# Performance work log

Measured on AMD Instinct MI355X. Metric: run time of the kernel, lower is better.

## Reference

```python
import jax, jax.numpy as jnp
import numpy as np

D_MODEL = 256
NUM_HEADS = 8
NUM_KV_HEADS = 4
HEAD_DIM = D_MODEL // NUM_HEADS
EPS = 1e-5


def layer_norm(x, g, b):
    mu = jnp.mean(x, axis=-1, keepdims=True)
    var = jnp.var(x, axis=-1, keepdims=True)
    return (x - mu) * jax.lax.rsqrt(var + EPS) * g + b


def gqa(x_q, x_kv, Wq, bq, Wk, bk, Wv, bv, Wo, bo):
    # x_q, x_kv: [BC, S, D]
    BC, S, D = x_q.shape
    G = NUM_HEADS // NUM_KV_HEADS
    q = (x_q @ Wq + bq).reshape(BC, S, NUM_HEADS, HEAD_DIM)
    k = (x_kv @ Wk + bk).reshape(BC, S, NUM_KV_HEADS, HEAD_DIM)
    v = (x_kv @ Wv + bv).reshape(BC, S, NUM_KV_HEADS, HEAD_DIM)
    # repeat_interleave over head dim to expand KV heads to query heads
    k = jnp.repeat(k, G, axis=2)
    v = jnp.repeat(v, G, axis=2)
    scale = 1.0 / np.sqrt(HEAD_DIM).astype(np.float32)
    scores = jnp.einsum('bqhd,bkhd->bhqk', q, k) * scale  # [BC,H,S,S]
    attn = jax.nn.softmax(scores, axis=-1)
    out = jnp.einsum('bhqk,bkhd->bqhd', attn, v).reshape(BC, S, D)
    return out @ Wo + bo


def _make_params(key):
    ks = jax.random.split(key, 20)
    D, Dkv = D_MODEL, NUM_KV_HEADS * HEAD_DIM
    s = 1.0 / np.sqrt(D).astype(np.float32)
    p = {}
    # 4 LayerNorms
    for name in ['spec_q', 'spec_kv', 'spat_q', 'spat_kv']:
        p[f'ln_{name}_g'] = jnp.ones((D,), jnp.float32)
        p[f'ln_{name}_b'] = jnp.zeros((D,), jnp.float32)
    # two GQA modules: s2t and t2s
    i = 0
    for tag in ['s2t', 't2s']:
        p[f'Wq_{tag}'] = jax.random.normal(ks[i], (D, D), jnp.float32) * s; i += 1
        p[f'bq_{tag}'] = jnp.zeros((D,), jnp.float32)
        p[f'Wk_{tag}'] = jax.random.normal(ks[i], (D, Dkv), jnp.float32) * s; i += 1
        p[f'bk_{tag}'] = jnp.zeros((Dkv,), jnp.float32)
        p[f'Wv_{tag}'] = jax.random.normal(ks[i], (D, Dkv), jnp.float32) * s; i += 1
        p[f'bv_{tag}'] = jnp.zeros((Dkv,), jnp.float32)
        p[f'Wo_{tag}'] = jax.random.normal(ks[i], (D, D), jnp.float32) * s; i += 1
        p[f'bo_{tag}'] = jnp.zeros((D,), jnp.float32)
    p['gate_spec'] = jnp.zeros((1,), jnp.float32)
    p['gate_spat'] = jnp.zeros((1,), jnp.float32)
    return p


def setup_inputs() -> dict:
    key = jax.random.key(0)
    k1, k2, k3 = jax.random.split(key, 3)
    B, S, C, D = 8, 64, 128, D_MODEL
    inp = {
        'x_spec': jax.random.normal(k1, (B, S, C, D), jnp.float32),
        'x_spat': jax.random.normal(k2, (B, S, C, D), jnp.float32),
    }
    inp.update(_make_params(k3))
    return inp


def reference(x_spec, x_spat,
              ln_spec_q_g, ln_spec_q_b, ln_spec_kv_g, ln_spec_kv_b,
              ln_spat_q_g, ln_spat_q_b, ln_spat_kv_g, ln_spat_kv_b,
              Wq_s2t, bq_s2t, Wk_s2t, bk_s2t, Wv_s2t, bv_s2t, Wo_s2t, bo_s2t,
              Wq_t2s, bq_t2s, Wk_t2s, bk_t2s, Wv_t2s, bv_t2s, Wo_t2s, bo_t2s,
              gate_spec, gate_spat):
    B, S, C, D = x_spec.shape
    # (B,S,C,D) -> (B*C, S, D)
    spec_flat = jnp.transpose(x_spec, (0, 2, 1, 3)).reshape(B * C, S, D)
    spat_flat = jnp.transpose(x_spat, (0, 2, 1, 3)).reshape(B * C, S, D)

    spec_q = layer_norm(spec_flat, ln_spec_q_g, ln_spec_q_b)
    spat_kv = layer_norm(spat_flat, ln_spat_kv_g, ln_spat_kv_b)
    delta_spec = gqa(spec_q, spat_kv, Wq_s2t, bq_s2t, Wk_s2t, bk_s2t, Wv_s2t, bv_s2t, Wo_s2t, bo_s2t)

    spat_q = layer_norm(spat_flat, ln_spat_q_g, ln_spat_q_b)
    spec_kv = layer_norm(spec_flat, ln_spec_kv_g, ln_spec_kv_b)
    delta_spat = gqa(spat_q, spec_kv, Wq_t2s, bq_t2s, Wk_t2s, bk_t2s, Wv_t2s, bv_t2s, Wo_t2s, bo_t2s)

    delta_spec = jnp.transpose(delta_spec.reshape(B, C, S, D), (0, 2, 1, 3))
    delta_spat = jnp.transpose(delta_spat.reshape(B, C, S, D), (0, 2, 1, 3))

    out_spec = x_spec + jax.nn.sigmoid(gate_spec) * delta_spec
    out_spat = x_spat + jax.nn.sigmoid(gate_spat) * delta_spat
    return (out_spec, out_spat)
```

## Files before the change

kernel.cpp:

```cpp
#include <hip/hip_runtime.h>

typedef short short8 __attribute__((ext_vector_type(8)));
typedef float f32x4 __attribute__((ext_vector_type(4)));

#define NELT 16777216

__device__ __forceinline__ float b2f(unsigned short u) {
    return __uint_as_float(((unsigned)u) << 16);
}
__device__ __forceinline__ unsigned short f2b(float f) {
    unsigned u = __float_as_uint(f);
    u += 0x7FFF + ((u >> 16) & 1);
    return (unsigned short)(u >> 16);
}
__device__ __forceinline__ void split2(float f, unsigned short& hi, unsigned short& lo) {
    unsigned short h = f2b(f);
    hi = h;
    lo = f2b(f - b2f(h));
}
__device__ __forceinline__ int xrow_off(int r) {
    int n = r >> 6, s = r & 63;
    int b = n >> 7, c = n & 127;
    return (((b << 6) + s) * 128 + c) << 8;
}
__device__ __forceinline__ int sw256(int row, int k) {
    return row * 256 + ((((k >> 3) ^ (row & 7)) << 3) | (k & 7));
}
__device__ __forceinline__ int boff(int nt, int kk, int ct, int lq, int lm) {
    return ((((nt * 8 + kk) * 4 + ct) * 4 + lq) * 16 + lm) * 16;
}

struct WArgs {
    const float* Wq[2]; const float* Wk[2]; const float* Wv[2]; const float* Wo[2];
    unsigned short* Bqkv[2]; unsigned short* Bo[2];
};
__global__ __launch_bounds__(256) void w_prep(WArgs A)
{
    const int dir = blockIdx.y;
    const int tid = blockIdx.x * 256 + threadIdx.x;
    const int lm = tid & 15, lq = (tid >> 4) & 3, ct = (tid >> 6) & 3;
    const int kk = (tid >> 8) & 7, nt = tid >> 11;
    const int c = ct * 16 + lm;
    {
        const float* W; int ldw, col;
        if (nt < 4)      { W = A.Wq[dir]; ldw = 256; col = nt * 64 + c; }
        else if (nt < 6) { W = A.Wk[dir]; ldw = 128; col = (nt - 4) * 64 + c; }
        else             { W = A.Wv[dir]; ldw = 128; col = (nt - 6) * 64 + c; }
        short8 h8, l8;
        #pragma unroll
        for (int j = 0; j < 8; ++j) {
            int k = kk * 32 + lq * 8 + j;
            unsigned short h, l;
            split2(W[k * ldw + col], h, l);
            h8[j] = (short)h; l8[j] = (short)l;
        }
        int off = boff(nt, kk, ct, lq, lm);
        *(short8*)&A.Bqkv[dir][off] = h8;
        *(short8*)&A.Bqkv[dir][off + 8] = l8;
    }
    if (nt < 4) {
        int col = nt * 64 + c;
        short8 h8, l8;
        #pragma unroll
        for (int j = 0; j < 8; ++j) {
            int k = kk * 32 + lq * 8 + j;
            unsigned short h, l;
            split2(A.Wo[dir][k * 256 + col], h, l);
            h8[j] = (short)h; l8[j] = (short)l;
        }
        int off = boff(nt, kk, ct, lq, lm);
        *(short8*)&A.Bo[dir][off] = h8;
        *(short8*)&A.Bo[dir][off + 8] = l8;
    }
}

struct FusedArgs {
    const float* xq[2];   const float* xkv[2];
    const float* gq[2];   const float* btq[2];
    const float* gkv[2];  const float* btkv[2];
    const unsigned short* Bqkv[2];
    const unsigned short* Bow[2];
    const float* bq[2];   const float* bk[2];
    const float* bv[2];   const float* bo[2];
    const float* gate[2];
    float* out[2];
};

__global__ __launch_bounds__(256, 2) void fused(FusedArgs P_)
{
    __shared__ char SM[40960];
    unsigned short* Ah = (unsigned short*)SM;
    unsigned short* Al = (unsigned short*)(SM + 16384);
    const int dir = blockIdx.y;
    const int n = blockIdx.x, t = threadIdx.x;
    const int r0 = n * 64;
    const int w = t >> 6, l = t & 63, lm = l & 15, lq = l >> 4;
    unsigned short* slot = (unsigned short*)(SM + w * 10240);

    const float* xq  = P_.xq[dir];
    const float* xkv = P_.xkv[dir];
    const unsigned short* Bq  = P_.Bqkv[dir];
    const unsigned short* BoW = P_.Bow[dir];

    auto stage_half = [&](const float* X, const float4& gv, const float4& b4, int h) {
        float4 xv[8];
        #pragma unroll
        for (int it = 0; it < 8; ++it)
            xv[it] = *(const float4*)(X + xrow_off(r0 + h * 32 + it * 4 + w) + l * 4);
        #pragma unroll
        for (int it = 0; it < 8; ++it) {
            int row = it * 4 + w;
            float4 x4 = xv[it];
            float s1 = x4.x + x4.y + x4.z + x4.w;
            float s2 = x4.x * x4.x + x4.y * x4.y + x4.z * x4.z + x4.w * x4.w;
            #pragma unroll
            for (int m = 1; m < 64; m <<= 1) {
                s1 += __shfl_xor(s1, m);
                s2 += __shfl_xor(s2, m);
            }
            float mu = s1 * (1.f / 256.f);
            float rstd = rsqrtf(s2 * (1.f / 256.f) - mu * mu + 1e-5f);
            float v0 = (x4.x - mu) * rstd * gv.x + b4.x;
            float v1 = (x4.y - mu) * rstd * gv.y + b4.y;
            float v2 = (x4.z - mu) * rstd * gv.z + b4.z;
            float v3 = (x4.w - mu) * rstd * gv.w + b4.w;
            ushort4 oh, ol;
            split2(v0, oh.x, ol.x); split2(v1, oh.y, ol.y);
            split2(v2, oh.z, ol.z); split2(v3, oh.w, ol.w);
            *(ushort4*)&Ah[sw256(row, l * 4)] = oh;
            *(ushort4*)&Al[sw256(row, l * 4)] = ol;
        }
    };

    f32x4 kacc[4][2] = {};
    f32x4 vacc[4][2] = {};
    {
        const float4 gv = *(const float4*)(P_.gkv[dir] + l * 4);
        const float4 b4 = *(const float4*)(P_.btkv[dir] + l * 4);
        const int ntK = 4 + (w >> 1), ntV = 6 + (w >> 1);
        #pragma unroll
        for (int h = 0; h < 2; ++h) {
            stage_half(xkv, gv, b4, h);
            __syncthreads();
            #pragma unroll
            for (int kk = 0; kk < 8; ++kk) {
                int k0 = kk * 32 + lq * 8;
                short8 ah[2], al[2];
                #pragma unroll
                for (int m2 = 0; m2 < 2; ++m2) {
                    ah[m2] = *(const short8*)&Ah[sw256(m2 * 16 + lm, k0)];
                    al[m2] = *(const short8*)&Al[sw256(m2 * 16 + lm, k0)];
                }
                #pragma unroll
                for (int i = 0; i < 2; ++i) {
                    int ct = (2 * w + i) & 3;
                    int offK = boff(ntK, kk, ct, lq, lm);
                    short8 bh = *(const short8*)&Bq[offK];
                    short8 bl = *(const short8*)&Bq[offK + 8];
                    #pragma unroll
                    for (int m2 = 0; m2 < 2; ++m2) {
                        int m = 2 * h + m2;
                        kacc[m][i] = __builtin_amdgcn_mfma_f32_16x16x32_bf16(ah[m2], bh, kacc[m][i], 0, 0, 0);
                        kacc[m][i] = __builtin_amdgcn_mfma_f32_16x16x32_bf16(al[m2], bh, kacc[m][i], 0, 0, 0);
                        kacc[m][i] = __builtin_amdgcn_mfma_f32_16x16x32_bf16(ah[m2], bl, kacc[m][i], 0, 0, 0);
                    }
                    int offV = boff(ntV, kk, ct, lq, lm);
                    bh = *(const short8*)&Bq[offV];
                    bl = *(const short8*)&Bq[offV + 8];
                    #pragma unroll
                    for (int m2 = 0; m2 < 2; ++m2) {
                        int m = 2 * h + m2;
                        vacc[m][i] = __builtin_amdgcn_mfma_f32_16x16x32_bf16(ah[m2], bh, vacc[m][i], 0, 0, 0);
                        vacc[m][i] = __builtin_amdgcn_mfma_f32_16x16x32_bf16(al[m2], bh, vacc[m][i], 0, 0, 0);
                        vacc[m][i] = __builtin_amdgcn_mfma_f32_16x16x32_bf16(ah[m2], bl, vacc[m][i], 0, 0, 0);
                    }
                }
            }
            __syncthreads();
        }
    }

    unsigned short* Ks = slot;
    unsigned short* Vs = slot + 2560;
    {
        float bkv0 = P_.bk[dir][w * 32 + lm],  bkv1 = P_.bk[dir][w * 32 + 16 + lm];
        float bvv0 = P_.bv[dir][w * 32 + lm],  bvv1 = P_.bv[dir][w * 32 + 16 + lm];
        #pragma unroll
        for (int m = 0; m < 4; ++m) {
            #pragma unroll
            for (int rg = 0; rg < 4; ++rg) {
                int key = m * 16 + lq * 4 + rg;
                Ks[key * 40 + lm]      = f2b(kacc[m][0][rg] + bkv0);
                Ks[key * 40 + 16 + lm] = f2b(kacc[m][1][rg] + bkv1);
                Vs[lm * 72 + key]        = f2b(vacc[m][0][rg] + bvv0);
                Vs[(16 + lm) * 72 + key] = f2b(vacc[m][1][rg] + bvv1);
            }
        }
    }
    short8 kf[4];
    #pragma unroll
    for (int nt = 0; nt < 4; ++nt)
        kf[nt] = *(const short8*)&Ks[(nt * 16 + lm) * 40 + lq * 8];
    short8 vb[2][2];
    #pragma unroll
    for (int kt = 0; kt < 2; ++kt) {
        vb[kt][0] = *(const short8*)&Vs[lm * 72 + kt * 32 + lq * 8];
        vb[kt][1] = *(const short8*)&Vs[(16 + lm) * 72 + kt * 32 + lq * 8];
    }
    __syncthreads();

    f32x4 qacc[4][4] = {};
    {
        const float4 gv = *(const float4*)(P_.gq[dir] + l * 4);
        const float4 b4 = *(const float4*)(P_.btq[dir] + l * 4);
        #pragma unroll
        for (int h = 0; h < 2; ++h) {
            stage_half(xq, gv, b4, h);
            __syncthreads();
            #pragma unroll
            for (int kk = 0; kk < 8; ++kk) {
                int k0 = kk * 32 + lq * 8;
                short8 ah[2], al[2];
                #pragma unroll
                for (int m2 = 0; m2 < 2; ++m2) {
                    ah[m2] = *(const short8*)&Ah[sw256(m2 * 16 + lm, k0)];
                    al[m2] = *(const short8*)&Al[sw256(m2 * 16 + lm, k0)];
                }
                #pragma unroll
                for (int i = 0; i < 4; ++i) {
                    int off = boff(w, kk, i, lq, lm);
                    short8 bh = *(const short8*)&Bq[off];
                    short8 bl = *(const short8*)&Bq[off + 8];
                    #pragma unroll
                    for (int m2 = 0; m2 < 2; ++m2) {
                        int m = 2 * h + m2;
                        qacc[m][i] = __builtin_amdgcn_mfma_f32_16x16x32_bf16(ah[m2], bh, qacc[m][i], 0, 0, 0);
                        qacc[m][i] = __builtin_amdgcn_mfma_f32_16x16x32_bf16(al[m2], bh, qacc[m][i], 0, 0, 0);
                        qacc[m][i] = __builtin_amdgcn_mfma_f32_16x16x32_bf16(ah[m2], bl, qacc[m][i], 0, 0, 0);
                    }
                }
            }
            __syncthreads();
        }
    }

    unsigned short* Qs = slot;
    {
        float bq0 = P_.bq[dir][w * 64 + lm],      bq1 = P_.bq[dir][w * 64 + 16 + lm];
        float bq2 = P_.bq[dir][w * 64 + 32 + lm], bq3 = P_.bq[dir][w * 64 + 48 + lm];
        #pragma unroll
        for (int m = 0; m < 4; ++m) {
            #pragma unroll
            for (int rg = 0; rg < 4; ++rg) {
                int row = (m * 16 + lq * 4 + rg) * 72;
                Qs[row + lm]      = f2b(qacc[m][0][rg] + bq0);
                Qs[row + 16 + lm] = f2b(qacc[m][1][rg] + bq1);
                Qs[row + 32 + lm] = f2b(qacc[m][2][rg] + bq2);
                Qs[row + 48 + lm] = f2b(qacc[m][3][rg] + bq3);
            }
        }
    }
    short8 qf[2][4];
    #pragma unroll
    for (int hi = 0; hi < 2; ++hi)
        #pragma unroll
        for (int mt = 0; mt < 4; ++mt)
            qf[hi][mt] = *(const short8*)&Qs[(mt * 16 + lm) * 72 + hi * 32 + lq * 8];

    unsigned short* Pw = slot;
    const float scale = 0.17677669529663687f;
    f32x4 o[2][4][2] = {};
    #pragma unroll
    for (int hi = 0; hi < 2; ++hi) {
        f32x4 s[4][4];
        #pragma unroll
        for (int mt = 0; mt < 4; ++mt) {
            #pragma unroll
            for (int nt = 0; nt < 4; ++nt) {
                f32x4 z = {0, 0, 0, 0};
                s[mt][nt] = __builtin_amdgcn_mfma_f32_16x16x32_bf16(qf[hi][mt], kf[nt], z, 0, 0, 0);
            }
        }
        #pragma unroll
        for (int mt = 0; mt < 4; ++mt) {
            #pragma unroll
            for (int rg = 0; rg < 4; ++rg) {
                float mx = fmaxf(fmaxf(s[mt][0][rg], s[mt][1][rg]),
                                 fmaxf(s[mt][2][rg], s[mt][3][rg]));
                #pragma unroll
                for (int msk = 1; msk < 16; msk <<= 1)
                    mx = fmaxf(mx, __shfl_xor(mx, msk));
                float p0 = __expf((s[mt][0][rg] - mx) * scale);
                float p1 = __expf((s[mt][1][rg] - mx) * scale);
                float p2 = __expf((s[mt][2][rg] - mx) * scale);
                float p3 = __expf((s[mt][3][rg] - mx) * scale);
                float sum = p0 + p1 + p2 + p3;
                #pragma unroll
                for (int msk = 1; msk < 16; msk <<= 1)
                    sum += __shfl_xor(sum, msk);
                float inv = 1.f / sum;
                int rowb = (mt * 16 + lq * 4 + rg) * 72 + lm;
                Pw[rowb + 0]  = f2b(p0 * inv);
                Pw[rowb + 16] = f2b(p1 * inv);
                Pw[rowb + 32] = f2b(p2 * inv);
                Pw[rowb + 48] = f2b(p3 * inv);
            }
        }
        #pragma unroll
        for (int kt = 0; kt < 2; ++kt) {
            #pragma unroll
            for (int mt = 0; mt < 4; ++mt) {
                short8 pa = *(const short8*)&Pw[(mt * 16 + lm) * 72 + kt * 32 + lq * 8];
                o[hi][mt][0] = __builtin_amdgcn_mfma_f32_16x16x32_bf16(pa, vb[kt][0], o[hi][mt][0], 0, 0, 0);
                o[hi][mt][1] = __builtin_amdgcn_mfma_f32_16x16x32_bf16(pa, vb[kt][1], o[hi][mt][1], 0, 0, 0);
            }
        }
    }
    __syncthreads();

    f32x4 acc[4][4] = {};
    #pragma unroll
    for (int h = 0; h < 2; ++h) {
        #pragma unroll
        for (int m2 = 0; m2 < 2; ++m2) {
            int mt = 2 * h + m2;
            #pragma unroll
            for (int hi = 0; hi < 2; ++hi) {
                #pragma unroll
                for (int n2 = 0; n2 < 2; ++n2) {
                    #pragma unroll
                    for (int rg = 0; rg < 4; ++rg) {
                        int row = m2 * 16 + lq * 4 + rg;
                        int col = w * 64 + hi * 32 + n2 * 16 + lm;
                        unsigned short h_, l_;
                        split2(o[hi][mt][n2][rg], h_, l_);
                        int sw = sw256(row, col);
                        Ah[sw] = h_;
                        Al[sw] = l_;
                    }
                }
            }
        }
        __syncthreads();
        #pragma unroll
        for (int kk = 0; kk < 8; ++kk) {
            int k0 = kk * 32 + lq * 8;
            short8 ah[2], al[2];
            #pragma unroll
            for (int m2 = 0; m2 < 2; ++m2) {
                ah[m2] = *(const short8*)&Ah[sw256(m2 * 16 + lm, k0)];
                al[m2] = *(const short8*)&Al[sw256(m2 * 16 + lm, k0)];
            }
            #pragma unroll
            for (int i = 0; i < 4; ++i) {
                int off = boff(w, kk, i, lq, lm);
                short8 bh = *(const short8*)&BoW[off];
                short8 bl = *(const short8*)&BoW[off + 8];
                #pragma unroll
                for (int m2 = 0; m2 < 2; ++m2) {
                    int m = 2 * h + m2;
                    acc[m][i] = __builtin_amdgcn_mfma_f32_16x16x32_bf16(ah[m2], bh, acc[m][i], 0, 0, 0);
                    acc[m][i] = __builtin_amdgcn_mfma_f32_16x16x32_bf16(al[m2], bh, acc[m][i], 0, 0, 0);
                    acc[m][i] = __builtin_amdgcn_mfma_f32_16x16x32_bf16(ah[m2], bl, acc[m][i], 0, 0, 0);
                }
            }
        }
        __syncthreads();
    }
    float sig = 1.f / (1.f + __expf(-P_.gate[dir][0]));
    const float* Xres = xq;
    float* Out = P_.out[dir];
    #pragma unroll
    for (int i = 0; i < 4; ++i) {
        int col = w * 64 + i * 16 + lm;
        float bias = P_.bo[dir][col];
        #pragma unroll
        for (int m = 0; m < 4; ++m) {
            #pragma unroll
            for (int rg = 0; rg < 4; ++rg) {
                int row = m * 16 + lq * 4 + rg;
                int oidx = xrow_off(r0 + row) + col;
                Out[oidx] = Xres[oidx] + sig * (acc[m][i][rg] + bias);
            }
        }
    }
}

extern "C" void kernel_launch(void* const* d_in, const int* in_sizes, int n_in,
                              void* d_out, int out_size, void* d_ws, size_t ws_size,
                              hipStream_t stream) {
    const float* x_spec = (const float*)d_in[0];
    const float* x_spat = (const float*)d_in[1];
    const float* ln_g[4] = {(const float*)d_in[2], (const float*)d_in[4],
                            (const float*)d_in[6], (const float*)d_in[8]};
    const float* ln_b[4] = {(const float*)d_in[3], (const float*)d_in[5],
                            (const float*)d_in[7], (const float*)d_in[9]};
    char* ws = (char*)d_ws;
    unsigned short* Bqkv[2] = {(unsigned short*)ws,
                               (unsigned short*)(ws + (512 << 10))};
    unsigned short* BoL[2]  = {(unsigned short*)(ws + (1024 << 10)),
                               (unsigned short*)(ws + (1280 << 10))};

    WArgs WA;
    for (int dir = 0; dir < 2; ++dir) {
        int base = 10 + dir * 8;
        WA.Wq[dir] = (const float*)d_in[base + 0];
        WA.Wk[dir] = (const float*)d_in[base + 2];
        WA.Wv[dir] = (const float*)d_in[base + 4];
        WA.Wo[dir] = (const float*)d_in[base + 6];
        WA.Bqkv[dir] = Bqkv[dir];
        WA.Bo[dir]   = BoL[dir];
    }
    w_prep<<<dim3(64, 2), 256, 0, stream>>>(WA);

    FusedArgs A;
    for (int dir = 0; dir < 2; ++dir) {
        int base = 10 + dir * 8;
        A.xq[dir]   = dir == 0 ? x_spec : x_spat;
        A.xkv[dir]  = dir == 0 ? x_spat : x_spec;
        A.gq[dir]   = dir == 0 ? ln_g[0] : ln_g[2];
        A.btq[dir]  = dir == 0 ? ln_b[0] : ln_b[2];
        A.gkv[dir]  = dir == 0 ? ln_g[3] : ln_g[1];
        A.btkv[dir] = dir == 0 ? ln_b[3] : ln_b[1];
        A.Bqkv[dir] = Bqkv[dir];
        A.Bow[dir]  = BoL[dir];
        A.bq[dir]   = (const float*)d_in[base + 1];
        A.bk[dir]   = (const float*)d_in[base + 3];
        A.bv[dir]   = (const float*)d_in[base + 5];
        A.bo[dir]   = (const float*)d_in[base + 7];
        A.gate[dir] = (const float*)d_in[26 + dir];
        A.out[dir]  = (float*)d_out + (size_t)dir * NELT;
    }
    fused<<<dim3(1024, 2), 256, 0, stream>>>(A);
}
```

Before: 562.4 us.

## Split work across eight waves per block, one head per wave

```diff
diff --git a/kernel.cpp b/kernel.cpp
--- a/kernel.cpp
+++ b/kernel.cpp
@@ -86,30 +86,29 @@
     float* out[2];
 };
 
-__global__ __launch_bounds__(256, 2) void fused(FusedArgs P_)
+__global__ __launch_bounds__(512, 4) void fused(FusedArgs P_)
 {
-    __shared__ char SM[40960];
+    __shared__ char SM[65536];
     unsigned short* Ah = (unsigned short*)SM;
-    unsigned short* Al = (unsigned short*)(SM + 16384);
+    unsigned short* Al = (unsigned short*)(SM + 32768);
     const int dir = blockIdx.y;
     const int n = blockIdx.x, t = threadIdx.x;
     const int r0 = n * 64;
     const int w = t >> 6, l = t & 63, lm = l & 15, lq = l >> 4;
-    unsigned short* slot = (unsigned short*)(SM + w * 10240);
 
     const float* xq  = P_.xq[dir];
     const float* xkv = P_.xkv[dir];
     const unsigned short* Bq  = P_.Bqkv[dir];
     const unsigned short* BoW = P_.Bow[dir];
 
-    auto stage_half = [&](const float* X, const float4& gv, const float4& b4, int h) {
+    auto stage = [&](const float* X, const float4& gv, const float4& b4) {
         float4 xv[8];
         #pragma unroll
         for (int it = 0; it < 8; ++it)
-            xv[it] = *(const float4*)(X + xrow_off(r0 + h * 32 + it * 4 + w) + l * 4);
+            xv[it] = *(const float4*)(X + xrow_off(r0 + it * 8 + w) + l * 4);
         #pragma unroll
         for (int it = 0; it < 8; ++it) {
-            int row = it * 4 + w;
+            int row = it * 8 + w;
             float4 x4 = xv[it];
             float s1 = x4.x + x4.y + x4.z + x4.w;
             float s2 = x4.x * x4.x + x4.y * x4.y + x4.z * x4.z + x4.w * x4.w;
@@ -131,257 +130,188 @@
             *(ushort4*)&Al[sw256(row, l * 4)] = ol;
         }
     };
-
-    f32x4 kacc[4][2] = {};
-    f32x4 vacc[4][2] = {};
+    auto gemm32 = [&](f32x4 (&acc)[4][2], const unsigned short* B,
+                      int nt, int ct0) {
+        #pragma unroll
+        for (int kk = 0; kk < 8; ++kk) {
+            int k0 = kk * 32 + lq * 8;
+            short8 ah[4], al[4];
+            #pragma unroll
+            for (int m = 0; m < 4; ++m) {
+                ah[m] = *(const short8*)&Ah[sw256(m * 16 + lm, k0)];
+                al[m] = *(const short8*)&Al[sw256(m * 16 + lm, k0)];
+            }
+            #pragma unroll
+            for (int i = 0; i < 2; ++i) {
+                int off = boff(nt, kk, ct0 + i, lq, lm);
+                short8 bh = *(const short8*)&B[off];
+                short8 bl = *(const short8*)&B[off + 8];
+                #pragma unroll
+                for (int m = 0; m < 4; ++m) {
+                    acc[m][i] = __builtin_amdgcn_mfma_f32_16x16x32_bf16(ah[m], bh, acc[m][i], 0, 0, 0);
+                    acc[m][i] = __builtin_amdgcn_mfma_f32_16x16x32_bf16(al[m], bh, acc[m][i], 0, 0, 0);
+                    acc[m][i] = __builtin_amdgcn_mfma_f32_16x16x32_bf16(ah[m], bl, acc[m][i], 0, 0, 0);
+                }
+            }
+        }
+    };
+
     {
         const float4 gv = *(const float4*)(P_.gkv[dir] + l * 4);
         const float4 b4 = *(const float4*)(P_.btkv[dir] + l * 4);
-        const int ntK = 4 + (w >> 1), ntV = 6 + (w >> 1);
-        #pragma unroll
-        for (int h = 0; h < 2; ++h) {
-            stage_half(xkv, gv, b4, h);
-            __syncthreads();
-            #pragma unroll
-            for (int kk = 0; kk < 8; ++kk) {
-                int k0 = kk * 32 + lq * 8;
-                short8 ah[2], al[2];
-                #pragma unroll
-                for (int m2 = 0; m2 < 2; ++m2) {
-                    ah[m2] = *(const short8*)&Ah[sw256(m2 * 16 + lm, k0)];
-                    al[m2] = *(const short8*)&Al[sw256(m2 * 16 + lm, k0)];
+        stage(xkv, gv, b4);
+    }
+    __syncthreads();
+    {
+        f32x4 acc[4][2] = {};
+        const int wk = w & 3;
+        const bool isV = w >= 4;
+        const int nt = (isV ? 6 : 4) + (wk >> 1);
+        const int ct0 = (wk & 1) * 2;
+        gemm32(acc, Bq, nt, ct0);
+        __syncthreads();
+        const float* bias = isV ? P_.bv[dir] : P_.bk[dir];
+        float bi0 = bias[wk * 32 + lm], bi1 = bias[wk * 32 + 16 + lm];
+        if (!isV) {
+            unsigned short* Ks = (unsigned short*)(SM + wk * 5120);
+            #pragma unroll
+            for (int m = 0; m < 4; ++m)
+                #pragma unroll
+                for (int rg = 0; rg < 4; ++rg) {
+                    int key = m * 16 + lq * 4 + rg;
+                    Ks[key * 40 + lm]      = f2b(acc[m][0][rg] + bi0);
+                    Ks[key * 40 + 16 + lm] = f2b(acc[m][1][rg] + bi1);
                 }
-                #pragma unroll
-                for (int i = 0; i < 2; ++i) {
-                    int ct = (2 * w + i) & 3;
-                    int offK = boff(ntK, kk, ct, lq, lm);
-                    short8 bh = *(const short8*)&Bq[offK];
-                    short8 bl = *(const short8*)&Bq[offK + 8];
-                    #pragma unroll
-                    for (int m2 = 0; m2 < 2; ++m2) {
-                        int m = 2 * h + m2;
-                        kacc[m][i] = __builtin_amdgcn_mfma_f32_16x16x32_bf16(ah[m2], bh, kacc[m][i], 0, 0, 0);
-                        kacc[m][i] = __builtin_amdgcn_mfma_f32_16x16x32_bf16(al[m2], bh, kacc[m][i], 0, 0, 0);
-                        kacc[m][i] = __builtin_amdgcn_mfma_f32_16x16x32_bf16(ah[m2], bl, kacc[m][i], 0, 0, 0);
-                    }
-                    int offV = boff(ntV, kk, ct, lq, lm);
-                    bh = *(const short8*)&Bq[offV];
-                    bl = *(const short8*)&Bq[offV + 8];
-                    #pragma unroll
-                    for (int m2 = 0; m2 < 2; ++m2) {
-                        int m = 2 * h + m2;
-                        vacc[m][i] = __builtin_amdgcn_mfma_f32_16x16x32_bf16(ah[m2], bh, vacc[m][i], 0, 0, 0);
-                        vacc[m][i] = __builtin_amdgcn_mfma_f32_16x16x32_bf16(al[m2], bh, vacc[m][i], 0, 0, 0);
-                        vacc[m][i] = __builtin_amdgcn_mfma_f32_16x16x32_bf16(ah[m2], bl, vacc[m][i], 0, 0, 0);
-                    }
+        } else {
+            unsigned short* Vs = (unsigned short*)(SM + 20480 + wk * 4608);
+            #pragma unroll
+            for (int m = 0; m < 4; ++m)
+                #pragma unroll
+                for (int rg = 0; rg < 4; ++rg) {
+                    int key = m * 16 + lq * 4 + rg;
+                    Vs[lm * 72 + key]        = f2b(acc[m][0][rg] + bi0);
+                    Vs[(16 + lm) * 72 + key] = f2b(acc[m][1][rg] + bi1);
                 }
-            }
-            __syncthreads();
-        }
-    }
-
-    unsigned short* Ks = slot;
-    unsigned short* Vs = slot + 2560;
-    {
-        float bkv0 = P_.bk[dir][w * 32 + lm],  bkv1 = P_.bk[dir][w * 32 + 16 + lm];
-        float bvv0 = P_.bv[dir][w * 32 + lm],  bvv1 = P_.bv[dir][w * 32 + 16 + lm];
-        #pragma unroll
-        for (int m = 0; m < 4; ++m) {
-            #pragma unroll
-            for (int rg = 0; rg < 4; ++rg) {
-                int key = m * 16 + lq * 4 + rg;
-                Ks[key * 40 + lm]      = f2b(kacc[m][0][rg] + bkv0);
-                Ks[key * 40 + 16 + lm] = f2b(kacc[m][1][rg] + bkv1);
-                Vs[lm * 72 + key]        = f2b(vacc[m][0][rg] + bvv0);
-                Vs[(16 + lm) * 72 + key] = f2b(vacc[m][1][rg] + bvv1);
-            }
-        }
-    }
+        }
+    }
+    __syncthreads();
+
+    const int g2 = w >> 1;
     short8 kf[4];
-    #pragma unroll
-    for (int nt = 0; nt < 4; ++nt)
-        kf[nt] = *(const short8*)&Ks[(nt * 16 + lm) * 40 + lq * 8];
+    {
+        const unsigned short* Ks = (const unsigned short*)(SM + g2 * 5120);
+        #pragma unroll
+        for (int nt = 0; nt < 4; ++nt)
+            kf[nt] = *(const short8*)&Ks[(nt * 16 + lm) * 40 + lq * 8];
+    }
     short8 vb[2][2];
-    #pragma unroll
-    for (int kt = 0; kt < 2; ++kt) {
-        vb[kt][0] = *(const short8*)&Vs[lm * 72 + kt * 32 + lq * 8];
-        vb[kt][1] = *(const short8*)&Vs[(16 + lm) * 72 + kt * 32 + lq * 8];
-    }
-    __syncthreads();
-
-    f32x4 qacc[4][4] = {};
+    {
+        const unsigned short* Vs = (const unsigned short*)(SM + 20480 + g2 * 4608);
+        #pragma unroll
+        for (int kt = 0; kt < 2; ++kt) {
+            vb[kt][0] = *(const short8*)&Vs[lm * 72 + kt * 32 + lq * 8];
+            vb[kt][1] = *(const short8*)&Vs[(16 + lm) * 72 + kt * 32 + lq * 8];
+        }
+    }
+    __syncthreads();
+
     {
         const float4 gv = *(const float4*)(P_.gq[dir] + l * 4);
         const float4 b4 = *(const float4*)(P_.btq[dir] + l * 4);
-        #pragma unroll
-        for (int h = 0; h < 2; ++h) {
-            stage_half(xq, gv, b4, h);
-            __syncthreads();
-            #pragma unroll
-            for (int kk = 0; kk < 8; ++kk) {
-                int k0 = kk * 32 + lq * 8;
-                short8 ah[2], al[2];
-                #pragma unroll
-                for (int m2 = 0; m2 < 2; ++m2) {
-                    ah[m2] = *(const short8*)&Ah[sw256(m2 * 16 + lm, k0)];
-                    al[m2] = *(const short8*)&Al[sw256(m2 * 16 + lm, k0)];
-                }
-                #pragma unroll
-                for (int i = 0; i < 4; ++i) {
-                    int off = boff(w, kk, i, lq, lm);
-                    short8 bh = *(const short8*)&Bq[off];
-                    short8 bl = *(const short8*)&Bq[off + 8];
-                    #pragma unroll
-                    for (int m2 = 0; m2 < 2; ++m2) {
-                        int m = 2 * h + m2;
-                        qacc[m][i] = __builtin_amdgcn_mfma_f32_16x16x32_bf16(ah[m2], bh, qacc[m][i], 0, 0, 0);
-                        qacc[m][i] = __builtin_amdgcn_mfma_f32_16x16x32_bf16(al[m2], bh, qacc[m][i], 0, 0, 0);
-                        qacc[m][i] = __builtin_amdgcn_mfma_f32_16x16x32_bf16(ah[m2], bl, qacc[m][i], 0, 0, 0);
-                    }
-                }
-            }
-            __syncthreads();
-        }
-    }
-
-    unsigned short* Qs = slot;
-    {
-        float bq0 = P_.bq[dir][w * 64 + lm],      bq1 = P_.bq[dir][w * 64 + 16 + lm];
-        float bq2 = P_.bq[dir][w * 64 + 32 + lm], bq3 = P_.bq[dir][w * 64 + 48 + lm];
-        #pragma unroll
-        for (int m = 0; m < 4; ++m) {
+        stage(xq, gv, b4);
+    }
+    __syncthreads();
+    f32x4 o[4][2] = {};
+    {
+        f32x4 qacc[4][2] = {};
+        gemm32(qacc, Bq, w >> 1, (w & 1) * 2);
+        __syncthreads();
+        unsigned short* Qs = (unsigned short*)(SM + w * 5120);
+        float bq0 = P_.bq[dir][w * 32 + lm], bq1 = P_.bq[dir][w * 32 + 16 + lm];
+        #pragma unroll
+        for (int m = 0; m < 4; ++m)
             #pragma unroll
             for (int rg = 0; rg < 4; ++rg) {
-                int row = (m * 16 + lq * 4 + rg) * 72;
+                int row = (m * 16 + lq * 4 + rg) * 40;
                 Qs[row + lm]      = f2b(qacc[m][0][rg] + bq0);
                 Qs[row + 16 + lm] = f2b(qacc[m][1][rg] + bq1);
-                Qs[row + 32 + lm] = f2b(qacc[m][2][rg] + bq2);
-                Qs[row + 48 + lm] = f2b(qacc[m][3][rg] + bq3);
-            }
-        }
-    }
-    short8 qf[2][4];
-    #pragma unroll
-    for (int hi = 0; hi < 2; ++hi)
-        #pragma unroll
-        for (int mt = 0; mt < 4; ++mt)
-            qf[hi][mt] = *(const short8*)&Qs[(mt * 16 + lm) * 72 + hi * 32 + lq * 8];
-
-    unsigned short* Pw = slot;
-    const float scale = 0.17677669529663687f;
-    f32x4 o[2][4][2] = {};
-    #pragma unroll
-    for (int hi = 0; hi < 2; ++hi) {
-        f32x4 s[4][4];
-        #pragma unroll
+            }
+        unsigned short* Ps = (unsigned short*)(SM + 40960 + w * 2304);
+        const float scale = 0.17677669529663687f;
+        #pragma unroll 1
         for (int mt = 0; mt < 4; ++mt) {
+            short8 qf = *(const short8*)&Qs[(mt * 16 + lm) * 40 + lq * 8];
+            f32x4 s[4];
             #pragma unroll
             for (int nt = 0; nt < 4; ++nt) {
                 f32x4 z = {0, 0, 0, 0};
-                s[mt][nt] = __builtin_amdgcn_mfma_f32_16x16x32_bf16(qf[hi][mt], kf[nt], z, 0, 0, 0);
-            }
-        }
-        #pragma unroll
-        for (int mt = 0; mt < 4; ++mt) {
+                s[nt] = __builtin_amdgcn_mfma_f32_16x16x32_bf16(qf, kf[nt], z, 0, 0, 0);
+            }
             #pragma unroll
             for (int rg = 0; rg < 4; ++rg) {
-                float mx = fmaxf(fmaxf(s[mt][0][rg], s[mt][1][rg]),
-                                 fmaxf(s[mt][2][rg], s[mt][3][rg]));
+                float mx = fmaxf(fmaxf(s[0][rg], s[1][rg]),
+                                 fmaxf(s[2][rg], s[3][rg]));
                 #pragma unroll
                 for (int msk = 1; msk < 16; msk <<= 1)
                     mx = fmaxf(mx, __shfl_xor(mx, msk));
-                float p0 = __expf((s[mt][0][rg] - mx) * scale);
-                float p1 = __expf((s[mt][1][rg] - mx) * scale);
-                float p2 = __expf((s[mt][2][rg] - mx) * scale);
-                float p3 = __expf((s[mt][3][rg] - mx) * scale);
+                float p0 = __expf((s[0][rg] - mx) * scale);
+                float p1 = __expf((s[1][rg] - mx) * scale);
+                float p2 = __expf((s[2][rg] - mx) * scale);
+                float p3 = __expf((s[3][rg] - mx) * scale);
                 float sum = p0 + p1 + p2 + p3;
                 #pragma unroll
                 for (int msk = 1; msk < 16; msk <<= 1)
                     sum += __shfl_xor(sum, msk);
                 float inv = 1.f / sum;
-                int rowb = (mt * 16 + lq * 4 + rg) * 72 + lm;
-                Pw[rowb + 0]  = f2b(p0 * inv);
-                Pw[rowb + 16] = f2b(p1 * inv);
-                Pw[rowb + 32] = f2b(p2 * inv);
-                Pw[rowb + 48] = f2b(p3 * inv);
-            }
-        }
-        #pragma unroll
-        for (int kt = 0; kt < 2; ++kt) {
-            #pragma unroll
-            for (int mt = 0; mt < 4; ++mt) {
-                short8 pa = *(const short8*)&Pw[(mt * 16 + lm) * 72 + kt * 32 + lq * 8];
-                o[hi][mt][0] = __builtin_amdgcn_mfma_f32_16x16x32_bf16(pa, vb[kt][0], o[hi][mt][0], 0, 0, 0);
-                o[hi][mt][1] = __builtin_amdgcn_mfma_f32_16x16x32_bf16(pa, vb[kt][1], o[hi][mt][1], 0, 0, 0);
-            }
-        }
-    }
-    __syncthreads();
-
-    f32x4 acc[4][4] = {};
+                int rowb = (lq * 4 + rg) * 72 + lm;
+                Ps[rowb + 0]  = f2b(p0 * inv);
+                Ps[rowb + 16] = f2b(p1 * inv);
+                Ps[rowb + 32] = f2b(p2 * inv);
+                Ps[rowb + 48] = f2b(p3 * inv);
+            }
+            #pragma unroll
+            for (int kt = 0; kt < 2; ++kt) {
+                short8 pa = *(const short8*)&Ps[lm * 72 + kt * 32 + lq * 8];
+                o[mt][0] = __builtin_amdgcn_mfma_f32_16x16x32_bf16(pa, vb[kt][0], o[mt][0], 0, 0, 0);
+                o[mt][1] = __builtin_amdgcn_mfma_f32_16x16x32_bf16(pa, vb[kt][1], o[mt][1], 0, 0, 0);
+            }
+        }
+    }
+    __syncthreads();
+
     #pragma unroll
-    for (int h = 0; h < 2; ++h) {
-        #pragma unroll
-        for (int m2 = 0; m2 < 2; ++m2) {
-            int mt = 2 * h + m2;
-            #pragma unroll
-            for (int hi = 0; hi < 2; ++hi) {
-                #pragma unroll
-                for (int n2 = 0; n2 < 2; ++n2) {
-                    #pragma unroll
-                    for (int rg = 0; rg < 4; ++rg) {
-                        int row = m2 * 16 + lq * 4 + rg;
-                        int col = w * 64 + hi * 32 + n2 * 16 + lm;
-                        unsigned short h_, l_;
-                        split2(o[hi][mt][n2][rg], h_, l_);
-                        int sw = sw256(row, col);
-                        Ah[sw] = h_;
-                        Al[sw] = l_;
-                    }
-                }
-            }
-        }
-        __syncthreads();
-        #pragma unroll
-        for (int kk = 0; kk < 8; ++kk) {
-            int k0 = kk * 32 + lq * 8;
-            short8 ah[2], al[2];
-            #pragma unroll
-            for (int m2 = 0; m2 < 2; ++m2) {
-                ah[m2] = *(const short8*)&Ah[sw256(m2 * 16 + lm, k0)];
-                al[m2] = *(const short8*)&Al[sw256(m2 * 16 + lm, k0)];
-            }
-            #pragma unroll
-            for (int i = 0; i < 4; ++i) {
-                int off = boff(w, kk, i, lq, lm);
-                short8 bh = *(const short8*)&BoW[off];
-                short8 bl = *(const short8*)&BoW[off + 8];
-                #pragma unroll
-                for (int m2 = 0; m2 < 2; ++m2) {
-                    int m = 2 * h + m2;
-                    acc[m][i] = __builtin_amdgcn_mfma_f32_16x16x32_bf16(ah[m2], bh, acc[m][i], 0, 0, 0);
-                    acc[m][i] = __builtin_amdgcn_mfma_f32_16x16x32_bf16(al[m2], bh, acc[m][i], 0, 0, 0);
-                    acc[m][i] = __builtin_amdgcn_mfma_f32_16x16x32_bf16(ah[m2], bl, acc[m][i], 0, 0, 0);
-                }
-            }
-        }
-        __syncthreads();
-    }
-    float sig = 1.f / (1.f + __expf(-P_.gate[dir][0]));
-    const float* Xres = xq;
-    float* Out = P_.out[dir];
-    #pragma unroll
-    for (int i = 0; i < 4; ++i) {
-        int col = w * 64 + i * 16 + lm;
-        float bias = P_.bo[dir][col];
-        #pragma unroll
-        for (int m = 0; m < 4; ++m) {
+    for (int m = 0; m < 4; ++m)
+        #pragma unroll
+        for (int n2 = 0; n2 < 2; ++n2)
             #pragma unroll
             for (int rg = 0; rg < 4; ++rg) {
                 int row = m * 16 + lq * 4 + rg;
-                int oidx = xrow_off(r0 + row) + col;
-                Out[oidx] = Xres[oidx] + sig * (acc[m][i][rg] + bias);
-            }
+                int col = w * 32 + n2 * 16 + lm;
+                unsigned short h_, l_;
+                split2(o[m][n2][rg], h_, l_);
+                int sw = sw256(row, col);
+                Ah[sw] = h_;
+                Al[sw] = l_;
+            }
+    __syncthreads();
+    {
+        f32x4 acc[4][2] = {};
+        gemm32(acc, BoW, w >> 1, (w & 1) * 2);
+        float sig = 1.f / (1.f + __expf(-P_.gate[dir][0]));
+        const float* Xres = xq;
+        float* Out = P_.out[dir];
+        #pragma unroll
+        for (int i = 0; i < 2; ++i) {
+            int col = w * 32 + i * 16 + lm;
+            float bias = P_.bo[dir][col];
+            #pragma unroll
+            for (int m = 0; m < 4; ++m)
+                #pragma unroll
+                for (int rg = 0; rg < 4; ++rg) {
+                    int row = m * 16 + lq * 4 + rg;
+                    int oidx = xrow_off(r0 + row) + col;
+                    Out[oidx] = Xres[oidx] + sig * (acc[m][i][rg] + bias);
+                }
         }
     }
 }
@@ -431,5 +361,5 @@
         A.gate[dir] = (const float*)d_in[26 + dir];
         A.out[dir]  = (float*)d_out + (size_t)dir * NELT;
     }
-    fused<<<dim3(1024, 2), 256, 0, stream>>>(A);
-}
+    fused<<<dim3(1024, 2), 512, 0, stream>>>(A);
+}
```

New measurement: 535.5 us. 1.05x faster.
